# Kernel tuning notes

Hardware: AMD Instinct MI355X
Metric: run time of the kernel (lower is better)

Reference implementation:

```python
import jax, jax.numpy as jnp
import numpy as np
from functools import partial

H = 768          # hidden_size (bert-base)
S = 256          # seq_len, forced by pool Linear(256*H -> H)
V = 30522        # vocab_size
NUM_TAGS = 2
B = 32


def _lstm_layer(x, w_ih, w_hh, b_ih, b_hh):
    # x: (B, S, I); torch weight layout: w_ih (4H, I), w_hh (4H, H), gate order i,f,g,o
    b, _, _ = x.shape
    h0 = jnp.zeros((b, H), x.dtype)
    c0 = jnp.zeros((b, H), x.dtype)
    bias = b_ih + b_hh

    def step(carry, xt):
        h, c = carry
        gates = xt @ w_ih.T + h @ w_hh.T + bias          # (B, 4H)
        i, f, g, o = jnp.split(gates, 4, axis=-1)
        i = jax.nn.sigmoid(i)
        f = jax.nn.sigmoid(f)
        g = jnp.tanh(g)
        o = jax.nn.sigmoid(o)
        c = f * c + i * g
        h = o * jnp.tanh(c)
        return (h, c), h

    _, hs = jax.lax.scan(step, (h0, c0), x.transpose(1, 0, 2))  # hs: (S, B, H)
    return hs.transpose(1, 0, 2)


def setup_inputs() -> dict:
    key = jax.random.key(0)
    ks = jax.random.split(key, 16)
    sc = 0.02
    inp = {
        "input_ids": jax.random.randint(ks[0], (B, S), 0, V, dtype=jnp.int32),
        "attention_mask": jnp.ones((B, S), jnp.int32),
        "token_type_ids": jnp.zeros((B, S), jnp.int32),
        "seq_label": jax.random.randint(ks[1], (B, NUM_TAGS), 0, 2, dtype=jnp.int32),
        "entity_ids": jax.random.randint(ks[2], (B, S), 0, 2, dtype=jnp.int32),
        "embed_table": jax.random.normal(ks[3], (V, H), jnp.float32) * sc,
        "w_ih0": jax.random.normal(ks[4], (4 * H, H), jnp.float32) * sc,
        "w_hh0": jax.random.normal(ks[5], (4 * H, H), jnp.float32) * sc,
        "b_ih0": jnp.zeros((4 * H,), jnp.float32),
        "b_hh0": jnp.zeros((4 * H,), jnp.float32),
        "w_ih1": jax.random.normal(ks[6], (4 * H, H), jnp.float32) * sc,
        "w_hh1": jax.random.normal(ks[7], (4 * H, H), jnp.float32) * sc,
        "b_ih1": jnp.zeros((4 * H,), jnp.float32),
        "b_hh1": jnp.zeros((4 * H,), jnp.float32),
        "pool_w": jax.random.normal(ks[8], (S * H, H), jnp.float32) * 0.002,
        "pool_b": jnp.zeros((H,), jnp.float32),
        "lin_w": jax.random.normal(ks[9], (H, NUM_TAGS), jnp.float32) * sc,
        "lin_b": jnp.zeros((NUM_TAGS,), jnp.float32),
    }
    return inp


def reference(input_ids, attention_mask, token_type_ids, seq_label, entity_ids,
              embed_table, w_ih0, w_hh0, b_ih0, b_hh0, w_ih1, w_hh1, b_ih1, b_hh1,
              pool_w, pool_b, lin_w, lin_b):
    x = embed_table[input_ids]                              # (B, S, H)
    out = _lstm_layer(x, w_ih0, w_hh0, b_ih0, b_hh0)        # layer 1
    out = _lstm_layer(out, w_ih1, w_hh1, b_ih1, b_hh1)      # layer 2 -> (B, S, H)

    seq_out = out.reshape(out.shape[0], -1) @ pool_w + pool_b   # (B, H)

    # batched version of the per-sample loop:
    # entity_out = tokens * (entity_ids == 1); concat seq_out row; global max over tokens
    mask = (entity_ids == 1).astype(out.dtype)[:, :, None]      # (B, S, 1)
    entity_out = out * mask                                     # (B, S, H)
    batch_out = jnp.maximum(entity_out.max(axis=1), seq_out)    # adaptive_max_pool1d(size=1)

    logits = batch_out @ lin_w + lin_b                          # (B, num_tags)

    # BCEWithLogitsLoss (dropout in eval mode = identity), numerically stable
    y = seq_label.astype(logits.dtype)
    loss = jnp.mean(jnp.maximum(logits, 0) - logits * y + jnp.log1p(jnp.exp(-jnp.abs(logits))))
    return (loss, logits)
```

## Files before the change

### kernel.cpp

```cpp
#include <hip/hip_runtime.h>
#include <hip/hip_bf16.h>
#include <stdint.h>

constexpr int Hh  = 768;
constexpr int Ss  = 256;
constexpr int Bb  = 32;
constexpr int G4  = 4 * Hh;
constexpr int MR  = Bb * Ss;
constexpr int NWGL = 96;
constexpr int NPOOL = 63;
constexpr int UPW8 = Hh / NWGL;
constexpr int LCW  = 4 * UPW8;
constexpr int FLS  = 8;

typedef short bf16x8 __attribute__((ext_vector_type(8)));
typedef float f32x4  __attribute__((ext_vector_type(4)));
typedef float f32x2  __attribute__((ext_vector_type(2)));

__device__ __forceinline__ unsigned short f2bf(float f) {
  union { float f; uint32_t u; } v; v.f = f;
  uint32_t u = v.u;
  return (unsigned short)((u + 0x7FFFu + ((u >> 16) & 1u)) >> 16);
}
__device__ __forceinline__ float bf2f(unsigned short h) {
  union { uint32_t u; float f; } v; v.u = ((uint32_t)h) << 16; return v.f;
}

__global__ __launch_bounds__(256) void k_embed(const int* __restrict__ ids,
                                               const float* __restrict__ table,
                                               unsigned short* __restrict__ x_bf) {
  int row = blockIdx.x;
  int id  = ids[row];
  const float* src = table + (size_t)id * Hh;
  unsigned short* dst = x_bf + (size_t)row * Hh;
  for (int j = threadIdx.x; j < Hh; j += 256) dst[j] = f2bf(src[j]);
}

__global__ __launch_bounds__(256) void k_cast(const float* __restrict__ src,
                                              unsigned short* __restrict__ dst, int n4) {
  int i = blockIdx.x * 256 + threadIdx.x;
  if (i < n4) {
    float4 v = ((const float4*)src)[i];
    uint2 o;
    o.x = (uint32_t)f2bf(v.x) | ((uint32_t)f2bf(v.y) << 16);
    o.y = (uint32_t)f2bf(v.z) | ((uint32_t)f2bf(v.w) << 16);
    ((uint2*)dst)[i] = o;
  }
}

__global__ __launch_bounds__(256) void k_gemm_bt(const unsigned short* __restrict__ A,
                                                 const unsigned short* __restrict__ Bw,
                                                 unsigned short* __restrict__ C,
                                                 const float* __restrict__ bias1,
                                                 const float* __restrict__ bias2,
                                                 int M, int N, int K) {
  constexpr int BM = 128, BN = 128, BK = 64;
  __shared__ unsigned short Asm[BM * BK];
  __shared__ unsigned short Bsm[BN * BK];
  const int tid = threadIdx.x, lane = tid & 63, wave = tid >> 6;
  const int m0 = blockIdx.x * BM, n0 = blockIdx.y * BN;
  const int wm = (wave & 1) * 64, wn = (wave >> 1) * 64;

  f32x4 acc[4][4];
  #pragma unroll
  for (int a = 0; a < 4; ++a)
    #pragma unroll
    for (int b = 0; b < 4; ++b) acc[a][b] = (f32x4){0.f, 0.f, 0.f, 0.f};

  const int nk = K / BK;
  bf16x8 ar[4], br[4];
  #pragma unroll
  for (int r = 0; r < 4; ++r) {
    int fb = r * 4096 + tid * 16;
    int row = fb >> 7;
    int kb  = (fb >> 4) & 7;
    ar[r] = *(const bf16x8*)(A  + (size_t)(m0 + row) * K + kb * 8);
    br[r] = *(const bf16x8*)(Bw + (size_t)(n0 + row) * K + kb * 8);
  }
  for (int it = 0; it < nk; ++it) {
    __syncthreads();
    #pragma unroll
    for (int r = 0; r < 4; ++r) {
      int fb = r * 4096 + tid * 16;
      int row = fb >> 7;
      int kb  = (fb >> 4) & 7;
      int sb  = kb ^ (row & 7);
      *(bf16x8*)((char*)Asm + row * 128 + sb * 16) = ar[r];
      *(bf16x8*)((char*)Bsm + row * 128 + sb * 16) = br[r];
    }
    __syncthreads();
    if (it + 1 < nk) {
      int k0 = (it + 1) * BK;
      #pragma unroll
      for (int r = 0; r < 4; ++r) {
        int fb = r * 4096 + tid * 16;
        int row = fb >> 7;
        int kb  = (fb >> 4) & 7;
        ar[r] = *(const bf16x8*)(A  + (size_t)(m0 + row) * K + k0 + kb * 8);
        br[r] = *(const bf16x8*)(Bw + (size_t)(n0 + row) * K + k0 + kb * 8);
      }
    }
    #pragma unroll
    for (int kk = 0; kk < 2; ++kk) {
      bf16x8 af[4], bfr[4];
      #pragma unroll
      for (int mi = 0; mi < 4; ++mi) {
        int row = wm + mi * 16 + (lane & 15);
        int kb  = kk * 4 + (lane >> 4);
        int sb  = kb ^ (row & 7);
        af[mi] = *(const bf16x8*)((const char*)Asm + row * 128 + sb * 16);
      }
      #pragma unroll
      for (int ni = 0; ni < 4; ++ni) {
        int row = wn + ni * 16 + (lane & 15);
        int kb  = kk * 4 + (lane >> 4);
        int sb  = kb ^ (row & 7);
        bfr[ni] = *(const bf16x8*)((const char*)Bsm + row * 128 + sb * 16);
      }
      #pragma unroll
      for (int mi = 0; mi < 4; ++mi)
        #pragma unroll
        for (int ni = 0; ni < 4; ++ni)
          acc[mi][ni] = __builtin_amdgcn_mfma_f32_16x16x32_bf16(af[mi], bfr[ni], acc[mi][ni], 0, 0, 0);
    }
  }
  #pragma unroll
  for (int mi = 0; mi < 4; ++mi)
    #pragma unroll
    for (int ni = 0; ni < 4; ++ni)
      #pragma unroll
      for (int r = 0; r < 4; ++r) {
        int row = m0 + wm + mi * 16 + (lane >> 4) * 4 + r;
        int col = wn + ni * 16 + (lane & 15);
        int bb = row >> 8, ss = row & 255;
        float v = acc[mi][ni][r] + bias1[n0 + col] + bias2[n0 + col];
        C[((size_t)ss * Bb + bb) * N + n0 + col] = f2bf(v);
      }
}

__global__ __launch_bounds__(256) void k_lstm2(
    const unsigned short* __restrict__ g_bf,
    const unsigned short* __restrict__ w_hh0b,
    const unsigned short* __restrict__ w_ih1b,
    const unsigned short* __restrict__ w_hh1b,
    const float* __restrict__ b_ih1,
    const float* __restrict__ b_hh1,
    unsigned short* __restrict__ hseq1,
    unsigned short* __restrict__ hseq2,
    const float* __restrict__ pool_w,
    float* __restrict__ partial,
    unsigned int* __restrict__ sync) {
  __shared__ __align__(16) char smem[2 * LCW * Hh * 2 + Bb * 33 * 4];
  unsigned short* Whh = (unsigned short*)smem;
  unsigned short* Wih = (unsigned short*)(smem + LCW * Hh * 2);
  float (*gsm)[33] = (float(*)[33])(smem + 2 * LCW * Hh * 2);

  const int wgid = blockIdx.x;
  const int tid = threadIdx.x;
  const int lane = tid & 63, w = tid >> 6;
  unsigned int* flags1 = sync;
  unsigned int* flags2 = sync + 96 * FLS;

  if (wgid >= 2 * NWGL) {
    const int p = wgid - 2 * NWGL;
    unsigned short* osm = (unsigned short*)smem;
    for (int s = p; s < Ss; s += NPOOL) {
      if (w == 0) {
        const unsigned need = (unsigned)(s + 1);
        for (;;) {
          unsigned fa = __hip_atomic_load(flags2 + lane * FLS, __ATOMIC_RELAXED, __HIP_MEMORY_SCOPE_AGENT);
          unsigned fb = __hip_atomic_load(flags2 + (64 + (lane & 31)) * FLS, __ATOMIC_RELAXED, __HIP_MEMORY_SCOPE_AGENT);
          if (__all(fa >= need) && __all(fb >= need)) break;
        }
      }
      __syncthreads();
      asm volatile("" ::: "memory");
      for (int b = 0; b < Bb; ++b) {
        const unsigned short* src = hseq2 + ((size_t)s * Bb + b) * Hh;
        for (int k = tid; k < Hh; k += 256) osm[k * Bb + b] = src[k];
      }
      __syncthreads();
      f32x2 acc[16][3];
      #pragma unroll
      for (int bp = 0; bp < 16; ++bp)
        #pragma unroll
        for (int j = 0; j < 3; ++j) acc[bp][j] = (f32x2){0.f, 0.f};
      const float* pbase = pool_w + (size_t)s * Hh * Hh;
      #pragma unroll 2
      for (int k = 0; k < Hh; ++k) {
        float w0 = pbase[(size_t)k * Hh + tid];
        float w1 = pbase[(size_t)k * Hh + 256 + tid];
        float w2 = pbase[(size_t)k * Hh + 512 + tid];
        const uint32_t* orow = (const uint32_t*)&osm[k * Bb];
        #pragma unroll
        for (int bp = 0; bp < 16; ++bp) {
          uint32_t pv = orow[bp];
          f32x2 ov;
          ov.x = __uint_as_float(pv << 16);
          ov.y = __uint_as_float(pv & 0xffff0000u);
          acc[bp][0] += ov * w0;
          acc[bp][1] += ov * w1;
          acc[bp][2] += ov * w2;
        }
      }
      float* pout = partial + (size_t)s * (Bb * Hh);
      #pragma unroll
      for (int bp = 0; bp < 16; ++bp)
        #pragma unroll
        for (int j = 0; j < 3; ++j) {
          pout[(size_t)(bp * 2 + 0) * Hh + j * 256 + tid] = acc[bp][j].x;
          pout[(size_t)(bp * 2 + 1) * Hh + j * 256 + tid] = acc[bp][j].y;
        }
      __syncthreads();
    }
    return;
  }

  const int layer = wgid >= NWGL;
  const int wg = layer ? wgid - NWGL : wgid;
  const int u0 = wg * UPW8;

  {
    const unsigned short* src = layer ? w_hh1b : w_hh0b;
    for (int cch = tid; cch < LCW * 96; cch += 256) {
      int row = cch / 96, kc = cch - row * 96;
      int gi = row >> 3, u = row & 7;
      *(bf16x8*)&Whh[row * Hh + ((kc ^ (row & 7)) * 8)] =
          *(const bf16x8*)(src + (size_t)(gi * Hh + u0 + u) * Hh + kc * 8);
    }
    if (layer) {
      for (int cch = tid; cch < LCW * 96; cch += 256) {
        int row = cch / 96, kc = cch - row * 96;
        int gi = row >> 3, u = row & 7;
        *(bf16x8*)&Wih[row * Hh + ((kc ^ (row & 7)) * 8)] =
            *(const bf16x8*)(w_ih1b + (size_t)(gi * Hh + u0 + u) * Hh + kc * 8);
      }
    }
  }
  __syncthreads();

  const int mtile = w & 1, nt2 = w >> 1;
  const int l15 = lane & 15, kq = lane >> 4;
  const int brow = mtile * 16 + l15;
  const int c = nt2 * 16 + l15;
  const int gi = c >> 3;
  const int gcol = gi * Hh + u0 + (c & 7);
  const float kmul = (gi == 2) ? 2.f : 1.f;
  const float amul = (gi == 2) ? 2.f : 1.f;
  const float aadd = (gi == 2) ? -1.f : 0.f;
  float bl = 0.f;
  if (layer) bl = b_ih1[gcol] + b_hh1[gcol];

  unsigned short gc[4];
  if (!layer) {
    #pragma unroll
    for (int r = 0; r < 4; ++r) {
      int b = mtile * 16 + kq * 4 + r;
      gc[r] = g_bf[(size_t)b * G4 + gcol];
    }
  }
  float cc[4] = {0.f, 0.f, 0.f, 0.f};
  unsigned short* hout = layer ? hseq2 : hseq1;
  unsigned int* myflag = (layer ? flags2 : flags1) + wg * FLS;

  for (int t = 0; t < Ss; ++t) {
    if (w == 0) {
      if (layer) {
        const unsigned need1 = (unsigned)(t + 1), need2 = (unsigned)t;
        for (;;) {
          unsigned f1a = __hip_atomic_load(flags1 + lane * FLS, __ATOMIC_RELAXED, __HIP_MEMORY_SCOPE_AGENT);
          unsigned f1b = __hip_atomic_load(flags1 + (64 + (lane & 31)) * FLS, __ATOMIC_RELAXED, __HIP_MEMORY_SCOPE_AGENT);
          unsigned f2a = __hip_atomic_load(flags2 + lane * FLS, __ATOMIC_RELAXED, __HIP_MEMORY_SCOPE_AGENT);
          unsigned f2b = __hip_atomic_load(flags2 + (64 + (lane & 31)) * FLS, __ATOMIC_RELAXED, __HIP_MEMORY_SCOPE_AGENT);
          if (__all(f1a >= need1) && __all(f1b >= need1) &&
              __all(f2a >= need2) && __all(f2b >= need2)) break;
        }
      } else if (t > 0) {
        const unsigned need = (unsigned)t;
        for (;;) {
          unsigned fa = __hip_atomic_load(flags1 + lane * FLS, __ATOMIC_RELAXED, __HIP_MEMORY_SCOPE_AGENT);
          unsigned fb = __hip_atomic_load(flags1 + (64 + (lane & 31)) * FLS, __ATOMIC_RELAXED, __HIP_MEMORY_SCOPE_AGENT);
          if (__all(fa >= need) && __all(fb >= need)) break;
        }
      }
    }
    __syncthreads();
    asm volatile("" ::: "memory");

    f32x4 a0 = {0.f, 0.f, 0.f, 0.f}, a1 = {0.f, 0.f, 0.f, 0.f};
    if (layer) {
      const unsigned short* ap = hseq1 + ((size_t)t * Bb + brow) * Hh + kq * 8;
      bf16x8 areg[24];
      #pragma unroll
      for (int kk = 0; kk < 24; ++kk) areg[kk] = *(const bf16x8*)(ap + kk * 32);
      #pragma unroll
      for (int kk = 0; kk < 24; ++kk) {
        bf16x8 bfr = *(const bf16x8*)&Wih[c * Hh + (((kk * 4 + kq) ^ (c & 7)) * 8)];
        if (kk & 1) a1 = __builtin_amdgcn_mfma_f32_16x16x32_bf16(areg[kk], bfr, a1, 0, 0, 0);
        else        a0 = __builtin_amdgcn_mfma_f32_16x16x32_bf16(areg[kk], bfr, a0, 0, 0, 0);
      }
    }
    if (t > 0) {
      const unsigned short* ap = hout + ((size_t)(t - 1) * Bb + brow) * Hh + kq * 8;
      bf16x8 areg[24];
      #pragma unroll
      for (int kk = 0; kk < 24; ++kk) areg[kk] = *(const bf16x8*)(ap + kk * 32);
      #pragma unroll
      for (int kk = 0; kk < 24; ++kk) {
        bf16x8 bfr = *(const bf16x8*)&Whh[c * Hh + (((kk * 4 + kq) ^ (c & 7)) * 8)];
        if (kk & 1) a1 = __builtin_amdgcn_mfma_f32_16x16x32_bf16(areg[kk], bfr, a1, 0, 0, 0);
        else        a0 = __builtin_amdgcn_mfma_f32_16x16x32_bf16(areg[kk], bfr, a0, 0, 0, 0);
      }
    }

    #pragma unroll
    for (int r = 0; r < 4; ++r) {
      float v = a0[r] + a1[r] + (layer ? bl : bf2f(gc[r]));
      float s = 1.f / (1.f + __expf(-kmul * v));
      gsm[mtile * 16 + kq * 4 + r][c] = amul * s + aadd;
    }
    if (!layer && w != 0 && t + 1 < Ss) {
      #pragma unroll
      for (int r = 0; r < 4; ++r) {
        int b = mtile * 16 + kq * 4 + r;
        gc[r] = g_bf[((size_t)(t + 1) * Bb + b) * G4 + gcol];
      }
    }
    __syncthreads();

    if (w == 0) {
      const int b = lane & 31, u4 = (lane >> 5) * 4;
      float hv[4];
      #pragma unroll
      for (int j = 0; j < 4; ++j) {
        const int u = u4 + j;
        float iv = gsm[b][u], fv = gsm[b][8 + u], gv = gsm[b][16 + u], ov = gsm[b][24 + u];
        float cn = fv * cc[j] + iv * gv;
        cc[j] = cn;
        float e = __expf(-2.f * cn);
        hv[j] = ov * (1.f - e) / (1.f + e);
      }
      uint32_t pk0 = (uint32_t)f2bf(hv[0]) | ((uint32_t)f2bf(hv[1]) << 16);
      uint32_t pk1 = (uint32_t)f2bf(hv[2]) | ((uint32_t)f2bf(hv[3]) << 16);
      uint32_t* hp = (uint32_t*)(hout + ((size_t)t * Bb + b) * Hh + u0 + u4);
      __hip_atomic_store(hp + 0, pk0, __ATOMIC_RELAXED, __HIP_MEMORY_SCOPE_AGENT);
      __hip_atomic_store(hp + 1, pk1, __ATOMIC_RELAXED, __HIP_MEMORY_SCOPE_AGENT);
      asm volatile("s_waitcnt vmcnt(0)" ::: "memory");
      if (lane == 0)
        __hip_atomic_store(myflag, (unsigned)(t + 1), __ATOMIC_RELAXED, __HIP_MEMORY_SCOPE_AGENT);
      if (!layer && t + 1 < Ss) {
        #pragma unroll
        for (int r = 0; r < 4; ++r) {
          int b2 = mtile * 16 + kq * 4 + r;
          gc[r] = g_bf[((size_t)(t + 1) * Bb + b2) * G4 + gcol];
        }
      }
    }
  }
}

__global__ __launch_bounds__(256) void k_pool_reduce(const float* __restrict__ partial,
                                                     const float* __restrict__ pool_b,
                                                     float* __restrict__ seq_out) {
  int i = blockIdx.x * 256 + threadIdx.x;
  float acc = pool_b[i % Hh];
  #pragma unroll 8
  for (int t = 0; t < Ss; ++t) acc += partial[(size_t)t * (Bb * Hh) + i];
  seq_out[i] = acc;
}

__global__ __launch_bounds__(256) void k_entity_logits(const unsigned short* __restrict__ hseq2,
                                                       const float* __restrict__ seq_out,
                                                       const int* __restrict__ entity_ids,
                                                       const float* __restrict__ lin_w,
                                                       const float* __restrict__ lin_b,
                                                       float* __restrict__ logits_ws,
                                                       float* __restrict__ dlogits) {
  const int b = blockIdx.x, tid = threadIdx.x;
  float m0 = -1e30f, m1 = -1e30f, m2 = -1e30f;
  for (int s = 0; s < Ss; ++s) {
    bool e = entity_ids[b * Ss + s] == 1;
    const unsigned short* row = hseq2 + ((size_t)s * Bb + b) * Hh;
    float v0 = bf2f(row[tid]);
    float v1 = bf2f(row[256 + tid]);
    float v2 = bf2f(row[512 + tid]);
    v0 = e ? v0 : 0.f; v1 = e ? v1 : 0.f; v2 = e ? v2 : 0.f;
    m0 = fmaxf(m0, v0); m1 = fmaxf(m1, v1); m2 = fmaxf(m2, v2);
  }
  __shared__ float red[512];
  float p0 = 0.f, p1 = 0.f;
  float mm[3] = {m0, m1, m2};
  #pragma unroll
  for (int j = 0; j < 3; ++j) {
    int n = j * 256 + tid;
    float bo = fmaxf(mm[j], seq_out[b * Hh + n]);
    p0 += bo * lin_w[n * 2 + 0];
    p1 += bo * lin_w[n * 2 + 1];
  }
  red[tid] = p0; red[256 + tid] = p1;
  __syncthreads();
  for (int off = 128; off > 0; off >>= 1) {
    if (tid < off) { red[tid] += red[tid + off]; red[256 + tid] += red[256 + tid + off]; }
    __syncthreads();
  }
  if (tid == 0) {
    float l0 = red[0] + lin_b[0], l1 = red[256] + lin_b[1];
    logits_ws[b * 2] = l0; logits_ws[b * 2 + 1] = l1;
    dlogits[b * 2] = l0;  dlogits[b * 2 + 1] = l1;
  }
}

__global__ void k_loss(const float* __restrict__ logits, const int* __restrict__ lab,
                       float* __restrict__ dout) {
  __shared__ float red[64];
  int i = threadIdx.x;
  float l = logits[i];
  float y = (float)lab[i];
  red[i] = fmaxf(l, 0.f) - l * y + log1pf(__expf(-fabsf(l)));
  __syncthreads();
  for (int off = 32; off > 0; off >>= 1) {
    if (i < off) red[i] += red[i + off];
    __syncthreads();
  }
  if (i == 0) dout[0] = red[0] * (1.f / 64.f);
}

extern "C" void kernel_launch(void* const* d_in, const int* in_sizes, int n_in,
                              void* d_out, int out_size, void* d_ws, size_t ws_size,
                              hipStream_t stream) {
  const int*   input_ids  = (const int*)d_in[0];
  const int*   seq_label  = (const int*)d_in[3];
  const int*   entity_ids = (const int*)d_in[4];
  const float* embed      = (const float*)d_in[5];
  const float* w_ih0      = (const float*)d_in[6];
  const float* w_hh0      = (const float*)d_in[7];
  const float* b_ih0      = (const float*)d_in[8];
  const float* b_hh0      = (const float*)d_in[9];
  const float* w_ih1      = (const float*)d_in[10];
  const float* w_hh1      = (const float*)d_in[11];
  const float* b_ih1      = (const float*)d_in[12];
  const float* b_hh1      = (const float*)d_in[13];
  const float* pool_w     = (const float*)d_in[14];
  const float* pool_b     = (const float*)d_in[15];
  const float* lin_w      = (const float*)d_in[16];
  const float* lin_b      = (const float*)d_in[17];
  float* out = (float*)d_out;

  const size_t SZ_XO = (size_t)Bb * Ss * Hh * 2;
  const size_t SZ_W  = (size_t)G4 * Hh * 2;
  const size_t SZ_G  = (size_t)Bb * Ss * G4 * 2;
  char* ws = (char*)d_ws;
  size_t off = 0;
  unsigned short* x_bf   = (unsigned short*)(ws + off); off += SZ_XO;
  unsigned short* wb_ih0 = (unsigned short*)(ws + off); off += SZ_W;
  unsigned short* wb_hh0 = (unsigned short*)(ws + off); off += SZ_W;
  unsigned short* wb_ih1 = (unsigned short*)(ws + off); off += SZ_W;
  unsigned short* wb_hh1 = (unsigned short*)(ws + off); off += SZ_W;
  unsigned short* g_bf   = (unsigned short*)(ws + off); off += SZ_G;
  unsigned short* hseq1  = (unsigned short*)(ws + off); off += SZ_XO;
  unsigned short* hseq2  = (unsigned short*)(ws + off); off += SZ_XO;
  float*          seq_out= (float*)(ws + off);          off += (size_t)Bb * Hh * 4;
  float*          logits = (float*)(ws + off);          off += 1024;
  unsigned int*   syncb  = (unsigned int*)(ws + off);   off += 8192;
  float*          partial = (float*)ws;

  hipMemsetAsync(syncb, 0, 8192, stream);

  k_embed<<<Bb * Ss, 256, 0, stream>>>(input_ids, embed, x_bf);
  int n4 = (G4 * Hh) / 4;
  int cgrid = (n4 + 255) / 256;
  k_cast<<<cgrid, 256, 0, stream>>>(w_ih0, wb_ih0, n4);
  k_cast<<<cgrid, 256, 0, stream>>>(w_hh0, wb_hh0, n4);
  k_cast<<<cgrid, 256, 0, stream>>>(w_ih1, wb_ih1, n4);
  k_cast<<<cgrid, 256, 0, stream>>>(w_hh1, wb_hh1, n4);

  dim3 ggrid(MR / 128, G4 / 128);
  k_gemm_bt<<<ggrid, 256, 0, stream>>>(x_bf, wb_ih0, g_bf, b_ih0, b_hh0, MR, G4, Hh);

  k_lstm2<<<2 * NWGL + NPOOL, 256, 0, stream>>>(g_bf, wb_hh0, wb_ih1, wb_hh1,
                                                b_ih1, b_hh1, hseq1, hseq2,
                                                pool_w, partial, syncb);

  k_pool_reduce<<<(Bb * Hh) / 256, 256, 0, stream>>>(partial, pool_b, seq_out);
  k_entity_logits<<<Bb, 256, 0, stream>>>(hseq2, seq_out, entity_ids, lin_w, lin_b,
                                          logits, out + 1);
  k_loss<<<1, 64, 0, stream>>>(logits, seq_label, out);
}
```

Baseline: 2.724 ms.

## Split LSTM workgroups into independent waves with per-wave flags; move pool out

The recurrent kernel now runs two independent waves per workgroup. Each wave owns 16 batch rows and all 32 gate columns, and combines the gates in registers through lane shuffles instead of shared memory and __syncthreads. Every wave polls the dense flag array itself with s_sleep backoff and publishes its own flag, which removes the block barriers and single-wave polling from the per-step critical path. The pool GEMM that used to be fused in as extra workgroups now runs as a separate kernel after the recurrence. That gives up the overlap of pool work with the LSTM in exchange for less contention and a shorter serial step.

```diff
diff --git a/kernel.cpp b/kernel.cpp
--- a/kernel.cpp
+++ b/kernel.cpp
@@ -8,10 +8,9 @@
 constexpr int G4  = 4 * Hh;
 constexpr int MR  = Bb * Ss;
 constexpr int NWGL = 96;
-constexpr int NPOOL = 63;
 constexpr int UPW8 = Hh / NWGL;
 constexpr int LCW  = 4 * UPW8;
-constexpr int FLS  = 8;
+constexpr int PB   = Bb + 2;
 
 typedef short bf16x8 __attribute__((ext_vector_type(8)));
 typedef float f32x4  __attribute__((ext_vector_type(4)));
@@ -138,7 +137,7 @@
       }
 }
 
-__global__ __launch_bounds__(256) void k_lstm2(
+__global__ __launch_bounds__(128) void k_lstm2(
     const unsigned short* __restrict__ g_bf,
     const unsigned short* __restrict__ w_hh0b,
     const unsigned short* __restrict__ w_ih1b,
@@ -147,74 +146,16 @@
     const float* __restrict__ b_hh1,
     unsigned short* __restrict__ hseq1,
     unsigned short* __restrict__ hseq2,
-    const float* __restrict__ pool_w,
-    float* __restrict__ partial,
     unsigned int* __restrict__ sync) {
-  __shared__ __align__(16) char smem[2 * LCW * Hh * 2 + Bb * 33 * 4];
-  unsigned short* Whh = (unsigned short*)smem;
-  unsigned short* Wih = (unsigned short*)(smem + LCW * Hh * 2);
-  float (*gsm)[33] = (float(*)[33])(smem + 2 * LCW * Hh * 2);
+  __shared__ __align__(16) unsigned short Whh[LCW * Hh];
+  __shared__ __align__(16) unsigned short Wih[LCW * Hh];
+  __shared__ __align__(16) unsigned short hbuf[2][16][8];
 
   const int wgid = blockIdx.x;
   const int tid = threadIdx.x;
   const int lane = tid & 63, w = tid >> 6;
   unsigned int* flags1 = sync;
-  unsigned int* flags2 = sync + 96 * FLS;
-
-  if (wgid >= 2 * NWGL) {
-    const int p = wgid - 2 * NWGL;
-    unsigned short* osm = (unsigned short*)smem;
-    for (int s = p; s < Ss; s += NPOOL) {
-      if (w == 0) {
-        const unsigned need = (unsigned)(s + 1);
-        for (;;) {
-          unsigned fa = __hip_atomic_load(flags2 + lane * FLS, __ATOMIC_RELAXED, __HIP_MEMORY_SCOPE_AGENT);
-          unsigned fb = __hip_atomic_load(flags2 + (64 + (lane & 31)) * FLS, __ATOMIC_RELAXED, __HIP_MEMORY_SCOPE_AGENT);
-          if (__all(fa >= need) && __all(fb >= need)) break;
-        }
-      }
-      __syncthreads();
-      asm volatile("" ::: "memory");
-      for (int b = 0; b < Bb; ++b) {
-        const unsigned short* src = hseq2 + ((size_t)s * Bb + b) * Hh;
-        for (int k = tid; k < Hh; k += 256) osm[k * Bb + b] = src[k];
-      }
-      __syncthreads();
-      f32x2 acc[16][3];
-      #pragma unroll
-      for (int bp = 0; bp < 16; ++bp)
-        #pragma unroll
-        for (int j = 0; j < 3; ++j) acc[bp][j] = (f32x2){0.f, 0.f};
-      const float* pbase = pool_w + (size_t)s * Hh * Hh;
-      #pragma unroll 2
-      for (int k = 0; k < Hh; ++k) {
-        float w0 = pbase[(size_t)k * Hh + tid];
-        float w1 = pbase[(size_t)k * Hh + 256 + tid];
-        float w2 = pbase[(size_t)k * Hh + 512 + tid];
-        const uint32_t* orow = (const uint32_t*)&osm[k * Bb];
-        #pragma unroll
-        for (int bp = 0; bp < 16; ++bp) {
-          uint32_t pv = orow[bp];
-          f32x2 ov;
-          ov.x = __uint_as_float(pv << 16);
-          ov.y = __uint_as_float(pv & 0xffff0000u);
-          acc[bp][0] += ov * w0;
-          acc[bp][1] += ov * w1;
-          acc[bp][2] += ov * w2;
-        }
-      }
-      float* pout = partial + (size_t)s * (Bb * Hh);
-      #pragma unroll
-      for (int bp = 0; bp < 16; ++bp)
-        #pragma unroll
-        for (int j = 0; j < 3; ++j) {
-          pout[(size_t)(bp * 2 + 0) * Hh + j * 256 + tid] = acc[bp][j].x;
-          pout[(size_t)(bp * 2 + 1) * Hh + j * 256 + tid] = acc[bp][j].y;
-        }
-      __syncthreads();
-    }
-    return;
-  }
+  unsigned int* flags2 = sync + 192;
 
   const int layer = wgid >= NWGL;
   const int wg = layer ? wgid - NWGL : wgid;
@@ -222,14 +163,14 @@
 
   {
     const unsigned short* src = layer ? w_hh1b : w_hh0b;
-    for (int cch = tid; cch < LCW * 96; cch += 256) {
+    for (int cch = tid; cch < LCW * 96; cch += 128) {
       int row = cch / 96, kc = cch - row * 96;
       int gi = row >> 3, u = row & 7;
       *(bf16x8*)&Whh[row * Hh + ((kc ^ (row & 7)) * 8)] =
           *(const bf16x8*)(src + (size_t)(gi * Hh + u0 + u) * Hh + kc * 8);
     }
     if (layer) {
-      for (int cch = tid; cch < LCW * 96; cch += 256) {
+      for (int cch = tid; cch < LCW * 96; cch += 128) {
         int row = cch / 96, kc = cch - row * 96;
         int gi = row >> 3, u = row & 7;
         *(bf16x8*)&Wih[row * Hh + ((kc ^ (row & 7)) * 8)] =
@@ -239,65 +180,79 @@
   }
   __syncthreads();
 
-  const int mtile = w & 1, nt2 = w >> 1;
   const int l15 = lane & 15, kq = lane >> 4;
-  const int brow = mtile * 16 + l15;
-  const int c = nt2 * 16 + l15;
-  const int gi = c >> 3;
-  const int gcol = gi * Hh + u0 + (c & 7);
-  const float kmul = (gi == 2) ? 2.f : 1.f;
-  const float amul = (gi == 2) ? 2.f : 1.f;
-  const float aadd = (gi == 2) ? -1.f : 0.f;
-  float bl = 0.f;
-  if (layer) bl = b_ih1[gcol] + b_hh1[gcol];
-
-  unsigned short gc[4];
+  const int brow = w * 16 + l15;
+  const bool lo8 = (l15 < 8);
+
+  int gcol[2]; float bl[2];
+  #pragma unroll
+  for (int nt = 0; nt < 2; ++nt) {
+    int c = nt * 16 + l15;
+    gcol[nt] = (c >> 3) * Hh + u0 + (c & 7);
+    bl[nt] = layer ? (b_ih1[gcol[nt]] + b_hh1[gcol[nt]]) : 0.f;
+  }
+  const float k1 = lo8 ? 2.f : 1.f;
+  const float m1 = lo8 ? 2.f : 1.f;
+  const float d1 = lo8 ? -1.f : 0.f;
+
+  unsigned short gc[2][4];
   if (!layer) {
     #pragma unroll
-    for (int r = 0; r < 4; ++r) {
-      int b = mtile * 16 + kq * 4 + r;
-      gc[r] = g_bf[(size_t)b * G4 + gcol];
-    }
+    for (int nt = 0; nt < 2; ++nt)
+      #pragma unroll
+      for (int r = 0; r < 4; ++r)
+        gc[nt][r] = g_bf[(size_t)(w * 16 + kq * 4 + r) * G4 + gcol[nt]];
   }
   float cc[4] = {0.f, 0.f, 0.f, 0.f};
   unsigned short* hout = layer ? hseq2 : hseq1;
-  unsigned int* myflag = (layer ? flags2 : flags1) + wg * FLS;
+  unsigned int* myflag = (layer ? flags2 : flags1) + wg * 2 + w;
 
   for (int t = 0; t < Ss; ++t) {
-    if (w == 0) {
-      if (layer) {
-        const unsigned need1 = (unsigned)(t + 1), need2 = (unsigned)t;
-        for (;;) {
-          unsigned f1a = __hip_atomic_load(flags1 + lane * FLS, __ATOMIC_RELAXED, __HIP_MEMORY_SCOPE_AGENT);
-          unsigned f1b = __hip_atomic_load(flags1 + (64 + (lane & 31)) * FLS, __ATOMIC_RELAXED, __HIP_MEMORY_SCOPE_AGENT);
-          unsigned f2a = __hip_atomic_load(flags2 + lane * FLS, __ATOMIC_RELAXED, __HIP_MEMORY_SCOPE_AGENT);
-          unsigned f2b = __hip_atomic_load(flags2 + (64 + (lane & 31)) * FLS, __ATOMIC_RELAXED, __HIP_MEMORY_SCOPE_AGENT);
-          if (__all(f1a >= need1) && __all(f1b >= need1) &&
-              __all(f2a >= need2) && __all(f2b >= need2)) break;
+    if (layer) {
+      const unsigned need1 = (unsigned)(t + 1), need2 = (unsigned)t;
+      for (;;) {
+        unsigned a0 = __hip_atomic_load(flags1 + lane, __ATOMIC_RELAXED, __HIP_MEMORY_SCOPE_AGENT);
+        unsigned a1 = __hip_atomic_load(flags1 + 64 + lane, __ATOMIC_RELAXED, __HIP_MEMORY_SCOPE_AGENT);
+        unsigned a2 = __hip_atomic_load(flags1 + 128 + lane, __ATOMIC_RELAXED, __HIP_MEMORY_SCOPE_AGENT);
+        bool ok = a0 >= need1 && a1 >= need1 && a2 >= need1;
+        if (need2) {
+          unsigned b0 = __hip_atomic_load(flags2 + lane, __ATOMIC_RELAXED, __HIP_MEMORY_SCOPE_AGENT);
+          unsigned b1 = __hip_atomic_load(flags2 + 64 + lane, __ATOMIC_RELAXED, __HIP_MEMORY_SCOPE_AGENT);
+          unsigned b2 = __hip_atomic_load(flags2 + 128 + lane, __ATOMIC_RELAXED, __HIP_MEMORY_SCOPE_AGENT);
+          ok = ok && b0 >= need2 && b1 >= need2 && b2 >= need2;
         }
-      } else if (t > 0) {
-        const unsigned need = (unsigned)t;
-        for (;;) {
-          unsigned fa = __hip_atomic_load(flags1 + lane * FLS, __ATOMIC_RELAXED, __HIP_MEMORY_SCOPE_AGENT);
-          unsigned fb = __hip_atomic_load(flags1 + (64 + (lane & 31)) * FLS, __ATOMIC_RELAXED, __HIP_MEMORY_SCOPE_AGENT);
-          if (__all(fa >= need) && __all(fb >= need)) break;
-        }
-      }
-    }
-    __syncthreads();
-    asm volatile("" ::: "memory");
-
-    f32x4 a0 = {0.f, 0.f, 0.f, 0.f}, a1 = {0.f, 0.f, 0.f, 0.f};
+        if (__all(ok)) break;
+        __builtin_amdgcn_s_sleep(2);
+      }
+      asm volatile("" ::: "memory");
+    } else if (t > 0) {
+      const unsigned need = (unsigned)t;
+      for (;;) {
+        unsigned a0 = __hip_atomic_load(flags1 + lane, __ATOMIC_RELAXED, __HIP_MEMORY_SCOPE_AGENT);
+        unsigned a1 = __hip_atomic_load(flags1 + 64 + lane, __ATOMIC_RELAXED, __HIP_MEMORY_SCOPE_AGENT);
+        unsigned a2 = __hip_atomic_load(flags1 + 128 + lane, __ATOMIC_RELAXED, __HIP_MEMORY_SCOPE_AGENT);
+        if (__all(a0 >= need && a1 >= need && a2 >= need)) break;
+        __builtin_amdgcn_s_sleep(2);
+      }
+      asm volatile("" ::: "memory");
+    }
+
+    f32x4 acc[2][2];
+    acc[0][0] = (f32x4){0.f,0.f,0.f,0.f}; acc[0][1] = (f32x4){0.f,0.f,0.f,0.f};
+    acc[1][0] = (f32x4){0.f,0.f,0.f,0.f}; acc[1][1] = (f32x4){0.f,0.f,0.f,0.f};
     if (layer) {
       const unsigned short* ap = hseq1 + ((size_t)t * Bb + brow) * Hh + kq * 8;
       bf16x8 areg[24];
       #pragma unroll
       for (int kk = 0; kk < 24; ++kk) areg[kk] = *(const bf16x8*)(ap + kk * 32);
       #pragma unroll
-      for (int kk = 0; kk < 24; ++kk) {
-        bf16x8 bfr = *(const bf16x8*)&Wih[c * Hh + (((kk * 4 + kq) ^ (c & 7)) * 8)];
-        if (kk & 1) a1 = __builtin_amdgcn_mfma_f32_16x16x32_bf16(areg[kk], bfr, a1, 0, 0, 0);
-        else        a0 = __builtin_amdgcn_mfma_f32_16x16x32_bf16(areg[kk], bfr, a0, 0, 0, 0);
+      for (int nt = 0; nt < 2; ++nt) {
+        const int c = nt * 16 + l15;
+        #pragma unroll
+        for (int kk = 0; kk < 24; ++kk) {
+          bf16x8 bfr = *(const bf16x8*)&Wih[c * Hh + (((kk * 4 + kq) ^ (c & 7)) * 8)];
+          acc[nt][kk & 1] = __builtin_amdgcn_mfma_f32_16x16x32_bf16(areg[kk], bfr, acc[nt][kk & 1], 0, 0, 0);
+        }
       }
     }
     if (t > 0) {
@@ -306,57 +261,105 @@
       #pragma unroll
       for (int kk = 0; kk < 24; ++kk) areg[kk] = *(const bf16x8*)(ap + kk * 32);
       #pragma unroll
-      for (int kk = 0; kk < 24; ++kk) {
-        bf16x8 bfr = *(const bf16x8*)&Whh[c * Hh + (((kk * 4 + kq) ^ (c & 7)) * 8)];
-        if (kk & 1) a1 = __builtin_amdgcn_mfma_f32_16x16x32_bf16(areg[kk], bfr, a1, 0, 0, 0);
-        else        a0 = __builtin_amdgcn_mfma_f32_16x16x32_bf16(areg[kk], bfr, a0, 0, 0, 0);
-      }
-    }
-
+      for (int nt = 0; nt < 2; ++nt) {
+        const int c = nt * 16 + l15;
+        #pragma unroll
+        for (int kk = 0; kk < 24; ++kk) {
+          bf16x8 bfr = *(const bf16x8*)&Whh[c * Hh + (((kk * 4 + kq) ^ (c & 7)) * 8)];
+          acc[nt][kk & 1] = __builtin_amdgcn_mfma_f32_16x16x32_bf16(areg[kk], bfr, acc[nt][kk & 1], 0, 0, 0);
+        }
+      }
+    }
+
+    float act0[4], act1[4];
     #pragma unroll
     for (int r = 0; r < 4; ++r) {
-      float v = a0[r] + a1[r] + (layer ? bl : bf2f(gc[r]));
-      float s = 1.f / (1.f + __expf(-kmul * v));
-      gsm[mtile * 16 + kq * 4 + r][c] = amul * s + aadd;
-    }
-    if (!layer && w != 0 && t + 1 < Ss) {
-      #pragma unroll
-      for (int r = 0; r < 4; ++r) {
-        int b = mtile * 16 + kq * 4 + r;
-        gc[r] = g_bf[((size_t)(t + 1) * Bb + b) * G4 + gcol];
-      }
-    }
-    __syncthreads();
-
-    if (w == 0) {
-      const int b = lane & 31, u4 = (lane >> 5) * 4;
-      float hv[4];
-      #pragma unroll
-      for (int j = 0; j < 4; ++j) {
-        const int u = u4 + j;
-        float iv = gsm[b][u], fv = gsm[b][8 + u], gv = gsm[b][16 + u], ov = gsm[b][24 + u];
-        float cn = fv * cc[j] + iv * gv;
-        cc[j] = cn;
-        float e = __expf(-2.f * cn);
-        hv[j] = ov * (1.f - e) / (1.f + e);
-      }
-      uint32_t pk0 = (uint32_t)f2bf(hv[0]) | ((uint32_t)f2bf(hv[1]) << 16);
-      uint32_t pk1 = (uint32_t)f2bf(hv[2]) | ((uint32_t)f2bf(hv[3]) << 16);
-      uint32_t* hp = (uint32_t*)(hout + ((size_t)t * Bb + b) * Hh + u0 + u4);
-      __hip_atomic_store(hp + 0, pk0, __ATOMIC_RELAXED, __HIP_MEMORY_SCOPE_AGENT);
-      __hip_atomic_store(hp + 1, pk1, __ATOMIC_RELAXED, __HIP_MEMORY_SCOPE_AGENT);
-      asm volatile("s_waitcnt vmcnt(0)" ::: "memory");
-      if (lane == 0)
-        __hip_atomic_store(myflag, (unsigned)(t + 1), __ATOMIC_RELAXED, __HIP_MEMORY_SCOPE_AGENT);
-      if (!layer && t + 1 < Ss) {
+      float v0 = acc[0][0][r] + acc[0][1][r] + (layer ? bl[0] : bf2f(gc[0][r]));
+      act0[r] = 1.f / (1.f + __expf(-v0));
+      float v1 = acc[1][0][r] + acc[1][1][r] + (layer ? bl[1] : bf2f(gc[1][r]));
+      act1[r] = m1 / (1.f + __expf(-k1 * v1)) + d1;
+    }
+
+    #pragma unroll
+    for (int r = 0; r < 4; ++r) {
+      float p0 = __shfl_xor(act0[r], 8);
+      float p1 = __shfl_xor(act1[r], 8);
+      float iv = lo8 ? act0[r] : p0;
+      float fv = lo8 ? p0 : act0[r];
+      float gv = lo8 ? act1[r] : p1;
+      float ov = lo8 ? p1 : act1[r];
+      float cn = fv * cc[r] + iv * gv;
+      cc[r] = cn;
+      float e = __expf(-2.f * cn);
+      float hv = ov * (1.f - e) / (1.f + e);
+      if (lo8) hbuf[w][kq * 4 + r][l15] = f2bf(hv);
+    }
+    asm volatile("s_waitcnt lgkmcnt(0)" ::: "memory");
+
+    if (lane < 16) {
+      const unsigned long long* hb = (const unsigned long long*)&hbuf[w][lane][0];
+      unsigned long long x0 = hb[0], x1 = hb[1];
+      unsigned long long* hp =
+          (unsigned long long*)(hout + ((size_t)t * Bb + (w * 16 + lane)) * Hh + u0);
+      __hip_atomic_store(hp + 0, x0, __ATOMIC_RELAXED, __HIP_MEMORY_SCOPE_AGENT);
+      __hip_atomic_store(hp + 1, x1, __ATOMIC_RELAXED, __HIP_MEMORY_SCOPE_AGENT);
+    }
+    asm volatile("s_waitcnt vmcnt(0)" ::: "memory");
+    if (lane == 0)
+      __hip_atomic_store(myflag, (unsigned)(t + 1), __ATOMIC_RELAXED, __HIP_MEMORY_SCOPE_AGENT);
+
+    if (!layer && t + 1 < Ss) {
+      #pragma unroll
+      for (int nt = 0; nt < 2; ++nt)
         #pragma unroll
-        for (int r = 0; r < 4; ++r) {
-          int b2 = mtile * 16 + kq * 4 + r;
-          gc[r] = g_bf[((size_t)(t + 1) * Bb + b2) * G4 + gcol];
-        }
-      }
-    }
-  }
+        for (int r = 0; r < 4; ++r)
+          gc[nt][r] = g_bf[((size_t)(t + 1) * Bb + (w * 16 + kq * 4 + r)) * G4 + gcol[nt]];
+    }
+  }
+}
+
+__global__ __launch_bounds__(256) void k_pool_partial(const unsigned short* __restrict__ hseq2,
+                                                      const float* __restrict__ pw,
+                                                      float* __restrict__ partial) {
+  __shared__ unsigned short osm[Hh * PB];
+  const int tid = threadIdx.x;
+  const int s = blockIdx.x;
+  for (int b = 0; b < Bb; ++b) {
+    const unsigned short* src = hseq2 + ((size_t)s * Bb + b) * Hh;
+    for (int k = tid; k < Hh; k += 256) osm[k * PB + b] = src[k];
+  }
+  __syncthreads();
+  f32x2 acc[16][3];
+  #pragma unroll
+  for (int bp = 0; bp < 16; ++bp)
+    #pragma unroll
+    for (int j = 0; j < 3; ++j) acc[bp][j] = (f32x2){0.f, 0.f};
+  const float* pbase = pw + (size_t)s * Hh * Hh;
+  #pragma unroll 2
+  for (int k = 0; k < Hh; ++k) {
+    float w0 = pbase[(size_t)k * Hh + tid];
+    float w1 = pbase[(size_t)k * Hh + 256 + tid];
+    float w2 = pbase[(size_t)k * Hh + 512 + tid];
+    const uint32_t* orow = (const uint32_t*)&osm[k * PB];
+    #pragma unroll
+    for (int bp = 0; bp < 16; ++bp) {
+      uint32_t pv = orow[bp];
+      f32x2 ov;
+      ov.x = __uint_as_float(pv << 16);
+      ov.y = __uint_as_float(pv & 0xffff0000u);
+      acc[bp][0] += ov * w0;
+      acc[bp][1] += ov * w1;
+      acc[bp][2] += ov * w2;
+    }
+  }
+  float* pout = partial + (size_t)s * (Bb * Hh);
+  #pragma unroll
+  for (int bp = 0; bp < 16; ++bp)
+    #pragma unroll
+    for (int j = 0; j < 3; ++j) {
+      pout[(size_t)(bp * 2 + 0) * Hh + j * 256 + tid] = acc[bp][j].x;
+      pout[(size_t)(bp * 2 + 1) * Hh + j * 256 + tid] = acc[bp][j].y;
+    }
 }
 
 __global__ __launch_bounds__(256) void k_pool_reduce(const float* __restrict__ partial,
@@ -461,10 +464,10 @@
   unsigned short* hseq2  = (unsigned short*)(ws + off); off += SZ_XO;
   float*          seq_out= (float*)(ws + off);          off += (size_t)Bb * Hh * 4;
   float*          logits = (float*)(ws + off);          off += 1024;
-  unsigned int*   syncb  = (unsigned int*)(ws + off);   off += 8192;
+  unsigned int*   syncb  = (unsigned int*)(ws + off);   off += 4096;
   float*          partial = (float*)ws;
 
-  hipMemsetAsync(syncb, 0, 8192, stream);
+  hipMemsetAsync(syncb, 0, 4096, stream);
 
   k_embed<<<Bb * Ss, 256, 0, stream>>>(input_ids, embed, x_bf);
   int n4 = (G4 * Hh) / 4;
@@ -477,10 +480,10 @@
   dim3 ggrid(MR / 128, G4 / 128);
   k_gemm_bt<<<ggrid, 256, 0, stream>>>(x_bf, wb_ih0, g_bf, b_ih0, b_hh0, MR, G4, Hh);
 
-  k_lstm2<<<2 * NWGL + NPOOL, 256, 0, stream>>>(g_bf, wb_hh0, wb_ih1, wb_hh1,
-                                                b_ih1, b_hh1, hseq1, hseq2,
-                                                pool_w, partial, syncb);
-
+  k_lstm2<<<2 * NWGL, 128, 0, stream>>>(g_bf, wb_hh0, wb_ih1, wb_hh1,
+                                        b_ih1, b_hh1, hseq1, hseq2, syncb);
+
+  k_pool_partial<<<Ss, 256, 0, stream>>>(hseq2, pool_w, partial);
   k_pool_reduce<<<(Bb * Hh) / 256, 256, 0, stream>>>(partial, pool_b, seq_out);
   k_entity_logits<<<Bb, 256, 0, stream>>>(hseq2, seq_out, entity_ids, lin_w, lin_b,
                                           logits, out + 1);
```

Measured after the change: 3.183 ms. 16.9% more time.
